# Performance work log

Measured on AMD Instinct MI355X. Metric: run time of the kernel, lower is better.

The kernel has to match this reference:

```python
import jax, jax.numpy as jnp
import numpy as np

B, S, D, H, FF = 2, 2048, 1024, 16, 4096
HD = D // H
EPS = 1e-5


def _ln(x, g, b):
    m = jnp.mean(x, axis=-1, keepdims=True)
    v = jnp.mean((x - m) ** 2, axis=-1, keepdims=True)
    return (x - m) * jax.lax.rsqrt(v + EPS) * g + b


def _rope(x, cos, sin):
    # non-standard RoPE: split full d_model at half, rotate (pre head-split)
    half = x.shape[-1] // 2
    x1, x2 = x[..., :half], x[..., half:]
    return jnp.concatenate([x1 * cos - x2 * sin, x1 * sin + x2 * cos], axis=-1)


def _heads(x, b, s):
    return x.reshape(b, s, H, HD).transpose(0, 2, 1, 3)  # [b,h,s,hd]


def _attn(q, k, v):
    scores = jnp.einsum('bhqd,bhkd->bhqk', q, k) / jnp.sqrt(jnp.float32(HD))
    w = jax.nn.softmax(scores, axis=-1)
    return jnp.einsum('bhqk,bhkd->bhqd', w, v)


def setup_inputs() -> dict:
    key = jax.random.key(0)
    ks = jax.random.split(key, 32)
    sc = 0.02
    d = {
        'x': jax.random.normal(ks[0], (B, S, D), jnp.float32),
        'cond_emb': jax.random.normal(ks[1], (B, D), jnp.float32),
    }
    # proper RoPE tables over half_dim = D//2
    pos = np.arange(S)[:, None]
    inv = 1.0 / (10000.0 ** (np.arange(D // 2) / (D // 2)))
    ang = pos * inv[None, :]
    d['cos_pos'] = jnp.asarray(np.cos(ang), jnp.float32)
    d['sin_pos'] = jnp.asarray(np.sin(ang), jnp.float32)
    names = ['Wq', 'Wk', 'Wv', 'Wo', 'Wqc', 'Wkc', 'Wvc', 'Woc']
    for i, n in enumerate(names):
        d[n] = jax.random.normal(ks[2 + i], (D, D), jnp.float32) * sc
        d['b' + n[1:]] = jnp.zeros((D,), jnp.float32)
    d['W1'] = jax.random.normal(ks[12], (D, FF), jnp.float32) * sc
    d['b1'] = jnp.zeros((FF,), jnp.float32)
    d['W2'] = jax.random.normal(ks[13], (FF, D), jnp.float32) * sc
    d['b2'] = jnp.zeros((D,), jnp.float32)
    for i in (1, 2, 3):
        d[f'g{i}'] = jnp.ones((D,), jnp.float32)
        d[f'be{i}'] = jnp.zeros((D,), jnp.float32)
    return d


def reference(x, cond_emb, cos_pos, sin_pos,
              Wq, bq, Wk, bk, Wv, bv, Wo, bo,
              Wqc, bqc, Wkc, bkc, Wvc, bvc, Woc, boc,
              W1, b1, W2, b2, g1, be1, g2, be2, g3, be3):
    b, s, _ = x.shape
    # self-attention with RoPE applied on full d_model before head split
    residual = x
    xn = _ln(x, g1, be1)
    q = _rope(xn @ Wq + bq, cos_pos, sin_pos)
    k = _rope(xn @ Wk + bk, cos_pos, sin_pos)
    v = xn @ Wv + bv
    o = _attn(_heads(q, b, s), _heads(k, b, s), _heads(v, b, s))
    o = o.transpose(0, 2, 1, 3).reshape(b, s, D) @ Wo + bo
    x = residual + o
    # cross-attention with single-token context
    residual = x
    xn = _ln(x, g2, be2)
    cond = cond_emb[:, None, :]  # [b,1,D]
    qc = _heads(xn @ Wqc + bqc, b, s)
    kc = _heads(cond @ Wkc + bkc, b, 1)
    vc = _heads(cond @ Wvc + bvc, b, 1)
    oc = _attn(qc, kc, vc)
    oc = oc.transpose(0, 2, 1, 3).reshape(b, s, D) @ Woc + boc
    x = residual + oc
    # FFN (exact GELU)
    residual = x
    xn = _ln(x, g3, be3)
    h = jax.nn.gelu(xn @ W1 + b1, approximate=False)
    return residual + (h @ W2 + b2)
```

## Files before the change

kernel.cpp:

```cpp
#include <hip/hip_runtime.h>
#include <cmath>

#define B_  2
#define S_  2048
#define D_  1024
#define H_  16
#define HD_ 64
#define FF_ 4096
#define M_  4096

typedef __attribute__((ext_vector_type(8))) __bf16 bf16x8;
typedef __attribute__((ext_vector_type(4))) __bf16 bf16x4;
typedef __attribute__((ext_vector_type(4))) float  f32x4;

__device__ __forceinline__ void gload_lds16(void* lds, const void* g) {
    __builtin_amdgcn_global_load_lds(
        (const __attribute__((address_space(1))) unsigned int*)g,
        (__attribute__((address_space(3))) unsigned int*)lds,
        16, 0, 0);
}

#define FENCE() asm volatile("" ::: "memory")

__global__ __launch_bounds__(256)
void tcast(const float* __restrict__ src, __bf16* __restrict__ dst, int K, int N)
{
    __shared__ float t[32][33];
    int tx = threadIdx.x & 31, ty = threadIdx.x >> 5;
    int k0 = blockIdx.y * 32, n0 = blockIdx.x * 32;
#pragma unroll
    for (int i = 0; i < 4; ++i)
        t[ty + i * 8][tx] = src[(size_t)(k0 + ty + i * 8) * N + n0 + tx];
    __syncthreads();
#pragma unroll
    for (int i = 0; i < 4; ++i)
        dst[(size_t)(n0 + ty + i * 8) * K + k0 + tx] = (__bf16)t[tx][ty + i * 8];
}

__global__ __launch_bounds__(256)
void catb(const float* __restrict__ a, const float* __restrict__ b,
          const float* __restrict__ c, float* __restrict__ o)
{
    int i = blockIdx.x * 256 + threadIdx.x;
    o[i] = i < 1024 ? a[i] : (i < 2048 ? b[i - 1024] : c[i - 2048]);
}

__global__ __launch_bounds__(256)
void colgemv(const float* __restrict__ inp, const float* __restrict__ W,
             const float* __restrict__ bias, float* __restrict__ out, int K, int N)
{
    __shared__ float part[4][16];
    const int b = blockIdx.y;
    const int t = threadIdx.x;
    const int w = t >> 6, lane = t & 63;
    const int colIdx = lane & 15;
    const int col = blockIdx.x * 16 + colIdx;
    const int ks = w * 4 + (lane >> 4);
    const int kpt = K >> 4;
    const float* ip = inp + (size_t)b * K + ks * kpt;
    const float* wp = W + (size_t)ks * kpt * N + col;
    float acc = 0.f;
#pragma unroll 8
    for (int i = 0; i < kpt; ++i)
        acc += ip[i] * wp[(size_t)i * N];
    acc += __shfl_xor(acc, 16);
    acc += __shfl_xor(acc, 32);
    if (lane < 16) part[w][colIdx] = acc;
    __syncthreads();
    if (t < 16) {
        float r = part[0][t] + part[1][t] + part[2][t] + part[3][t]
                + bias[blockIdx.x * 16 + t];
        out[(size_t)b * N + blockIdx.x * 16 + t] = r;
    }
}

__global__ __launch_bounds__(256)
void ln_cast(const float* __restrict__ x, const float* __restrict__ g,
             const float* __restrict__ be, __bf16* __restrict__ out)
{
    int row = blockIdx.x, tid = threadIdx.x;
    const float4* xp = (const float4*)(x + (size_t)row * D_);
    float4 v = xp[tid];
    float s  = v.x + v.y + v.z + v.w;
    float s2 = v.x * v.x + v.y * v.y + v.z * v.z + v.w * v.w;
#pragma unroll
    for (int off = 32; off > 0; off >>= 1) {
        s  += __shfl_down(s, off);
        s2 += __shfl_down(s2, off);
    }
    __shared__ float rs[4], rs2[4];
    int wid = tid >> 6, lane = tid & 63;
    if (lane == 0) { rs[wid] = s; rs2[wid] = s2; }
    __syncthreads();
    float tot  = rs[0] + rs[1] + rs[2] + rs[3];
    float tot2 = rs2[0] + rs2[1] + rs2[2] + rs2[3];
    float mean = tot * (1.0f / D_);
    float var  = tot2 * (1.0f / D_) - mean * mean;
    float rstd = rsqrtf(var + 1e-5f);
    float4 gv = ((const float4*)g)[tid];
    float4 bv = ((const float4*)be)[tid];
    bf16x4 ov;
    ov[0] = (__bf16)((v.x - mean) * rstd * gv.x + bv.x);
    ov[1] = (__bf16)((v.y - mean) * rstd * gv.y + bv.y);
    ov[2] = (__bf16)((v.z - mean) * rstd * gv.z + bv.z);
    ov[3] = (__bf16)((v.w - mean) * rstd * gv.w + bv.w);
    ((bf16x4*)(out + (size_t)row * D_))[tid] = ov;
}

__global__ __launch_bounds__(128)
void rope2(const __bf16* __restrict__ qkv, const float* __restrict__ cosp,
           const float* __restrict__ sinp, __bf16* __restrict__ out,
           int off, float scale)
{
    int row = blockIdx.x, tid = threadIdx.x;
    int b = row >> 11, s = row & 2047;
    bf16x4 a  = *(const bf16x4*)(qkv + (size_t)row * 3072 + off + tid * 4);
    bf16x4 bb = *(const bf16x4*)(qkv + (size_t)row * 3072 + off + 512 + tid * 4);
    float4 c  = ((const float4*)(cosp + (size_t)s * 512))[tid];
    float4 sn = ((const float4*)(sinp + (size_t)s * 512))[tid];
    float x1a = (float)a[0],  x1b = (float)a[1],  x1c = (float)a[2],  x1d = (float)a[3];
    float x2a = (float)bb[0], x2b = (float)bb[1], x2c = (float)bb[2], x2d = (float)bb[3];
    int d0 = tid * 4;
    int h1 = d0 >> 6, dd = d0 & 63;
    bf16x4 o1, o2;
    o1[0] = (__bf16)((x1a * c.x - x2a * sn.x) * scale);
    o1[1] = (__bf16)((x1b * c.y - x2b * sn.y) * scale);
    o1[2] = (__bf16)((x1c * c.z - x2c * sn.z) * scale);
    o1[3] = (__bf16)((x1d * c.w - x2d * sn.w) * scale);
    o2[0] = (__bf16)((x1a * sn.x + x2a * c.x) * scale);
    o2[1] = (__bf16)((x1b * sn.y + x2b * c.y) * scale);
    o2[2] = (__bf16)((x1c * sn.z + x2c * c.z) * scale);
    o2[3] = (__bf16)((x1d * sn.w + x2d * c.w) * scale);
    *(bf16x4*)(out + ((size_t)((b * H_ + h1) * S_ + s) * HD_) + dd) = o1;
    *(bf16x4*)(out + ((size_t)((b * H_ + h1 + 8) * S_ + s) * HD_) + dd) = o2;
}

__global__ __launch_bounds__(256)
void vtrans2(const __bf16* __restrict__ qkv, __bf16* __restrict__ Vt)
{
    __shared__ __bf16 t[32][33];
    int tx = threadIdx.x & 31, ty = threadIdx.x >> 5;
    int bh = blockIdx.z;
    int b = bh >> 4, h = bh & 15;
    int s0 = blockIdx.y * 32, d0 = blockIdx.x * 32;
    __bf16* dst = Vt + (size_t)bh * HD_ * S_;
#pragma unroll
    for (int i = 0; i < 4; ++i)
        t[ty + i * 8][tx] = qkv[(size_t)(b * 2048 + s0 + ty + i * 8) * 3072
                                + 2048 + h * 64 + d0 + tx];
    __syncthreads();
#pragma unroll
    for (int i = 0; i < 4; ++i)
        dst[(size_t)(d0 + ty + i * 8) * S_ + s0 + tx] = t[tx][ty + i * 8];
}

template<int EPI>
__global__ __launch_bounds__(512)
void gemm8(const __bf16* __restrict__ A, const __bf16* __restrict__ Bt,
           const float* __restrict__ bias, __bf16* __restrict__ o0,
           __bf16* __restrict__ o1, int M, int N, int K, int klen)
{
    __shared__ __align__(16) char smem[131072];
    const int tid = threadIdx.x;
    const int wid = tid >> 6, lane = tid & 63;
    const int l15 = lane & 15, l16 = lane >> 4;
    const int wm = wid >> 2, wn = wid & 3;

    const int gx = gridDim.x;
    const int nwg = gx * gridDim.y;
    int wg = blockIdx.y * gx + blockIdx.x;
    wg = (wg & 7) * (nwg >> 3) + (wg >> 3);
    const int n0 = (wg % gx) * 256;
    const int m0 = (wg / gx) * 256;
    const int kz = blockIdx.z * klen;
    const size_t K2 = (size_t)K * 2;

    const int srow = tid >> 3;
    const int scol = ((tid & 7) * 16) ^ ((srow & 7) << 4);
    const char* gA = (const char*)A + (size_t)(m0 + srow) * K2 + (size_t)kz * 2 + scol;
    const char* gB = (const char*)Bt + (size_t)(n0 + srow) * K2 + (size_t)kz * 2 + scol;

    auto stageA = [&](int c) {
        char* d = (char*)smem + c * 32768 + wid * 1024;
        gload_lds16(d,         gA);
        gload_lds16(d + 8192,  gA + 64 * K2);
        gload_lds16(d + 16384, gA + 128 * K2);
        gload_lds16(d + 24576, gA + 192 * K2);
    };
    auto stageB = [&](int c) {
        char* d = (char*)smem + 65536 + c * 32768 + wid * 1024;
        gload_lds16(d,         gB);
        gload_lds16(d + 8192,  gB + 64 * K2);
        gload_lds16(d + 16384, gB + 128 * K2);
        gload_lds16(d + 24576, gB + 192 * K2);
    };

    const int sw = (l15 & 7) << 4;
    const int x0 = (l16 * 16) ^ sw;
    const int x1 = (64 + l16 * 16) ^ sw;
    const int aoff = (wm * 128 + l15) * 128;
    const int boff = 65536 + (wn * 64 + l15) * 128;

    f32x4 acc[8][4] = {};
    const int NT = klen >> 6;

    stageA(0); stageB(0); gA += 128; gB += 128;
    stageA(1); stageB(1); gA += 128; gB += 128;
    asm volatile("s_waitcnt vmcnt(8)" ::: "memory");
    __builtin_amdgcn_s_barrier();

    for (int t = 0; t < NT; ++t) {
        const int cur = t & 1;
        const char* sa = (const char*)smem + cur * 32768;
        const bool pf = (t + 2) < NT;

        bf16x8 af0[8], af1[8];
        bf16x8 b00, b01, b02, b03, b10, b11, b12, b13;

#pragma unroll
        for (int mi = 0; mi < 8; ++mi)
            af0[mi] = *(const bf16x8*)(sa + aoff + mi * 2048 + x0);
        b00 = *(const bf16x8*)(sa + boff + 0 * 2048 + x0);
        b01 = *(const bf16x8*)(sa + boff + 1 * 2048 + x0);
        FENCE();
        __builtin_amdgcn_s_barrier();
        __builtin_amdgcn_s_setprio(1);
#pragma unroll
        for (int mi = 0; mi < 8; ++mi) {
            acc[mi][0] = __builtin_amdgcn_mfma_f32_16x16x32_bf16(af0[mi], b00, acc[mi][0], 0, 0, 0);
            acc[mi][1] = __builtin_amdgcn_mfma_f32_16x16x32_bf16(af0[mi], b01, acc[mi][1], 0, 0, 0);
        }
        __builtin_amdgcn_s_setprio(0);

#pragma unroll
        for (int mi = 0; mi < 8; ++mi)
            af1[mi] = *(const bf16x8*)(sa + aoff + mi * 2048 + x1);
        b02 = *(const bf16x8*)(sa + boff + 2 * 2048 + x0);
        b03 = *(const bf16x8*)(sa + boff + 3 * 2048 + x0);
        FENCE();
        __builtin_amdgcn_s_barrier();
        __builtin_amdgcn_s_setprio(1);
#pragma unroll
        for (int mi = 0; mi < 8; ++mi) {
            acc[mi][2] = __builtin_amdgcn_mfma_f32_16x16x32_bf16(af0[mi], b02, acc[mi][2], 0, 0, 0);
            acc[mi][3] = __builtin_amdgcn_mfma_f32_16x16x32_bf16(af0[mi], b03, acc[mi][3], 0, 0, 0);
        }
        __builtin_amdgcn_s_setprio(0);

        b10 = *(const bf16x8*)(sa + boff + 0 * 2048 + x1);
        b11 = *(const bf16x8*)(sa + boff + 1 * 2048 + x1);
        FENCE();
        __builtin_amdgcn_s_barrier();
        if (pf) stageA(cur);
        __builtin_amdgcn_s_setprio(1);
#pragma unroll
        for (int mi = 0; mi < 8; ++mi) {
            acc[mi][0] = __builtin_amdgcn_mfma_f32_16x16x32_bf16(af1[mi], b10, acc[mi][0], 0, 0, 0);
            acc[mi][1] = __builtin_amdgcn_mfma_f32_16x16x32_bf16(af1[mi], b11, acc[mi][1], 0, 0, 0);
        }
        __builtin_amdgcn_s_setprio(0);

        b12 = *(const bf16x8*)(sa + boff + 2 * 2048 + x1);
        b13 = *(const bf16x8*)(sa + boff + 3 * 2048 + x1);
        FENCE();
        __builtin_amdgcn_s_barrier();
        if (pf) { stageB(cur); gA += 128; gB += 128; }
        __builtin_amdgcn_s_setprio(1);
#pragma unroll
        for (int mi = 0; mi < 8; ++mi) {
            acc[mi][2] = __builtin_amdgcn_mfma_f32_16x16x32_bf16(af1[mi], b12, acc[mi][2], 0, 0, 0);
            acc[mi][3] = __builtin_amdgcn_mfma_f32_16x16x32_bf16(af1[mi], b13, acc[mi][3], 0, 0, 0);
        }
        __builtin_amdgcn_s_setprio(0);
        if (pf) asm volatile("s_waitcnt vmcnt(8)" ::: "memory");
        else    asm volatile("s_waitcnt vmcnt(0)" ::: "memory");
        __builtin_amdgcn_s_barrier();
        FENCE();
    }

#pragma unroll
    for (int mi = 0; mi < 8; ++mi)
#pragma unroll
        for (int ni = 0; ni < 4; ++ni) {
            int gc = n0 + wn * 64 + ni * 16 + l15;
            float bb = (EPI == 2) ? 0.f : bias[gc];
#pragma unroll
            for (int r = 0; r < 4; ++r) {
                int gr = m0 + wm * 128 + mi * 16 + l16 * 4 + r;
                float v = acc[mi][ni][r] + bb;
                if constexpr (EPI == 0) {
                    o0[(size_t)gr * N + gc] = (__bf16)v;
                } else if constexpr (EPI == 1) {
                    o0[(size_t)gr * N + gc] =
                        (__bf16)(0.5f * v * (1.0f + erff(v * 0.70710678118f)));
                } else {
                    const size_t PSZ = (size_t)M_ * 1024;
                    __bf16* po = (blockIdx.z < 2) ? (o0 + blockIdx.z * PSZ)
                                                  : (o1 + (blockIdx.z - 2) * PSZ);
                    po[(size_t)gr * N + gc] = (__bf16)v;
                }
            }
        }
}

__global__ __launch_bounds__(256)
void ffn2_red(const __bf16* __restrict__ pA, const __bf16* __restrict__ pB,
              const float* __restrict__ x2, const float* __restrict__ b2,
              float* __restrict__ out)
{
    const size_t PSZ = (size_t)M_ * 1024;
    size_t i = ((size_t)blockIdx.x * 256 + threadIdx.x) * 8;
    bf16x8 a0 = *(const bf16x8*)(pA + i);
    bf16x8 a1 = *(const bf16x8*)(pA + PSZ + i);
    bf16x8 c0 = *(const bf16x8*)(pB + i);
    bf16x8 c1 = *(const bf16x8*)(pB + PSZ + i);
    float4 xa = *(const float4*)(x2 + i);
    float4 xb = *(const float4*)(x2 + i + 4);
    float xs[8] = {xa.x, xa.y, xa.z, xa.w, xb.x, xb.y, xb.z, xb.w};
#pragma unroll
    for (int j = 0; j < 8; ++j) {
        int col = (int)((i + j) & 1023);
        out[i + j] = xs[j] + b2[col]
                   + (float)a0[j] + (float)a1[j] + (float)c0[j] + (float)c1[j];
    }
}

__global__ __launch_bounds__(256)
void gemm_bt(const __bf16* __restrict__ A, const __bf16* __restrict__ Bt,
             const float* __restrict__ bias, const float* __restrict__ resid,
             const float* __restrict__ extra, float* __restrict__ outF,
             int M, int N, int K)
{
    __shared__ __align__(16) __bf16 As[128 * 64];
    __shared__ __align__(16) __bf16 Bs[128 * 64];
    const int tid = threadIdx.x;
    const int wid = tid >> 6, lane = tid & 63;
    const int m0 = blockIdx.y * 128, n0 = blockIdx.x * 128;
    const int wm = wid >> 1, wn = wid & 1;
    const int l15 = lane & 15, l16 = lane >> 4;

    f32x4 acc[4][4] = {};
    char* asb = (char*)As;
    char* bsb = (char*)Bs;
    const char* ag = (const char*)A;
    const char* bg = (const char*)Bt;
    const int srow = lane >> 3;
    const int scolsw = ((lane & 7) * 16) ^ (srow << 4);

    for (int k0 = 0; k0 < K; k0 += 64) {
        __syncthreads();
#pragma unroll
        for (int i = 0; i < 4; ++i) {
            int j = wid * 4 + i;
            int row = j * 8 + srow;
            gload_lds16(asb + j * 1024,
                        ag + (size_t)(m0 + row) * (K * 2) + k0 * 2 + scolsw);
        }
#pragma unroll
        for (int i = 0; i < 4; ++i) {
            int j = wid * 4 + i;
            int row = j * 8 + srow;
            gload_lds16(bsb + j * 1024,
                        bg + (size_t)(n0 + row) * (K * 2) + k0 * 2 + scolsw);
        }
        __syncthreads();

        bf16x8 af[4][2], bfr[4][2];
#pragma unroll
        for (int mi = 0; mi < 4; ++mi) {
            int row = wm * 64 + mi * 16 + l15;
            int swl = (row & 7) << 4;
#pragma unroll
            for (int kk = 0; kk < 2; ++kk)
                af[mi][kk] = *(const bf16x8*)(asb + row * 128 + ((l16 * 16 + kk * 64) ^ swl));
        }
#pragma unroll
        for (int ni = 0; ni < 4; ++ni) {
            int row = wn * 64 + ni * 16 + l15;
            int swl = (row & 7) << 4;
#pragma unroll
            for (int kk = 0; kk < 2; ++kk)
                bfr[ni][kk] = *(const bf16x8*)(bsb + row * 128 + ((l16 * 16 + kk * 64) ^ swl));
        }
#pragma unroll
        for (int mi = 0; mi < 4; ++mi)
#pragma unroll
            for (int ni = 0; ni < 4; ++ni) {
                acc[mi][ni] = __builtin_amdgcn_mfma_f32_16x16x32_bf16(af[mi][0], bfr[ni][0], acc[mi][ni], 0, 0, 0);
                acc[mi][ni] = __builtin_amdgcn_mfma_f32_16x16x32_bf16(af[mi][1], bfr[ni][1], acc[mi][ni], 0, 0, 0);
            }
    }

#pragma unroll
    for (int mi = 0; mi < 4; ++mi)
#pragma unroll
        for (int ni = 0; ni < 4; ++ni) {
            int gc = n0 + wn * 64 + ni * 16 + l15;
            float bb = bias[gc];
#pragma unroll
            for (int r = 0; r < 4; ++r) {
                int gr = m0 + wm * 64 + mi * 16 + l16 * 4 + r;
                float v = acc[mi][ni][r] + bb;
                size_t idx = (size_t)gr * N + gc;
                int b = gr >> 11;
                outF[idx] = resid[idx] + v + extra[(size_t)b * N + gc];
            }
        }
}

__global__ __launch_bounds__(256)
void attn_fwd(const __bf16* __restrict__ Qh, const __bf16* __restrict__ Kh,
              const __bf16* __restrict__ Vt, __bf16* __restrict__ O)
{
    __shared__ __align__(16) char smem[24576];
    char* Kl = smem;
    char* Vl = smem + 8192;
    char* Pl = smem + 16384;
    const int tid = threadIdx.x, wid = tid >> 6, lane = tid & 63;
    const int l15 = lane & 15, l16 = lane >> 4;
    const int bh = blockIdx.y;
    const int q0 = blockIdx.x * 64 + wid * 16;
    const size_t qkbase = (size_t)bh * S_ * HD_;

    bf16x8 qf[2];
    {
        const __bf16* qp = Qh + qkbase + (size_t)(q0 + l15) * HD_ + l16 * 8;
        qf[0] = *(const bf16x8*)qp;
        qf[1] = *(const bf16x8*)(qp + 32);
    }
    float m = -1e30f, sum = 0.f;
    f32x4 o[4] = {};
    const int srow = lane >> 3;
    const int scolsw = ((lane & 7) * 16) ^ (srow << 4);
    const char* kg = (const char*)(Kh + qkbase);
    const char* vg = (const char*)(Vt + (size_t)bh * HD_ * S_);

    for (int kt = 0; kt < S_ / 64; ++kt) {
        int s0 = kt * 64;
        __syncthreads();
#pragma unroll
        for (int c = 0; c < 2; ++c) {
            int j = wid * 2 + c;
            int row = j * 8 + srow;
            gload_lds16(Kl + j * 1024, kg + (size_t)(s0 + row) * 128 + scolsw);
            gload_lds16(Vl + j * 1024, vg + (size_t)row * (S_ * 2) + s0 * 2 + scolsw);
        }
        __syncthreads();

        f32x4 st[4];
#pragma unroll
        for (int t = 0; t < 4; ++t) {
            int row = t * 16 + l15;
            int swl = (row & 7) << 4;
            bf16x8 ak0 = *(const bf16x8*)(Kl + row * 128 + ((l16 * 16) ^ swl));
            bf16x8 ak1 = *(const bf16x8*)(Kl + row * 128 + ((l16 * 16 + 64) ^ swl));
            f32x4 z = {0.f, 0.f, 0.f, 0.f};
            z = __builtin_amdgcn_mfma_f32_16x16x32_bf16(ak0, qf[0], z, 0, 0, 0);
            st[t] = __builtin_amdgcn_mfma_f32_16x16x32_bf16(ak1, qf[1], z, 0, 0, 0);
        }
        float rmax = -1e30f;
#pragma unroll
        for (int t = 0; t < 4; ++t)
#pragma unroll
            for (int r = 0; r < 4; ++r) rmax = fmaxf(rmax, st[t][r]);
        rmax = fmaxf(rmax, __shfl_xor(rmax, 16));
        rmax = fmaxf(rmax, __shfl_xor(rmax, 32));
        float mnew = fmaxf(m, rmax);
        float corr = __expf(m - mnew);
        float rsum = 0.f;
        float p[4][4];
#pragma unroll
        for (int t = 0; t < 4; ++t)
#pragma unroll
            for (int r = 0; r < 4; ++r) { p[t][r] = __expf(st[t][r] - mnew); rsum += p[t][r]; }
        rsum += __shfl_xor(rsum, 16);
        rsum += __shfl_xor(rsum, 32);
        sum = sum * corr + rsum;
        m = mnew;
        {
            char* pw = Pl + wid * 2048 + l15 * 128;
            int swl = (l15 & 7) << 4;
#pragma unroll
            for (int t = 0; t < 4; ++t) {
                bf16x4 pk;
                pk[0] = (__bf16)p[t][0]; pk[1] = (__bf16)p[t][1];
                pk[2] = (__bf16)p[t][2]; pk[3] = (__bf16)p[t][3];
                *(bf16x4*)(pw + ((t * 32 + l16 * 8) ^ swl)) = pk;
            }
        }
        float c0 = __shfl(corr, l16 * 4 + 0);
        float c1 = __shfl(corr, l16 * 4 + 1);
        float c2 = __shfl(corr, l16 * 4 + 2);
        float c3 = __shfl(corr, l16 * 4 + 3);
#pragma unroll
        for (int dg = 0; dg < 4; ++dg) {
            o[dg][0] *= c0; o[dg][1] *= c1; o[dg][2] *= c2; o[dg][3] *= c3;
        }
        {
            const char* pr = Pl + wid * 2048 + l15 * 128;
            int swp = (l15 & 7) << 4;
            bf16x8 ap0 = *(const bf16x8*)(pr + ((l16 * 16) ^ swp));
            bf16x8 ap1 = *(const bf16x8*)(pr + ((l16 * 16 + 64) ^ swp));
#pragma unroll
            for (int dg = 0; dg < 4; ++dg) {
                int row = dg * 16 + l15;
                int swl = (row & 7) << 4;
                bf16x8 bv0 = *(const bf16x8*)(Vl + row * 128 + ((l16 * 16) ^ swl));
                bf16x8 bv1 = *(const bf16x8*)(Vl + row * 128 + ((l16 * 16 + 64) ^ swl));
                o[dg] = __builtin_amdgcn_mfma_f32_16x16x32_bf16(ap0, bv0, o[dg], 0, 0, 0);
                o[dg] = __builtin_amdgcn_mfma_f32_16x16x32_bf16(ap1, bv1, o[dg], 0, 0, 0);
            }
        }
    }
    int b = bh >> 4, hh = bh & 15;
#pragma unroll
    for (int r = 0; r < 4; ++r) {
        float inv = 1.0f / __shfl(sum, l16 * 4 + r);
        int qg = q0 + l16 * 4 + r;
        __bf16* op = O + ((size_t)(b * S_ + qg) * D_) + hh * HD_;
#pragma unroll
        for (int dg = 0; dg < 4; ++dg)
            op[dg * 16 + l15] = (__bf16)(o[dg][r] * inv);
    }
}

extern "C" void kernel_launch(void* const* d_in, const int* in_sizes, int n_in,
                              void* d_out, int out_size, void* d_ws, size_t ws_size,
                              hipStream_t stream)
{
    (void)in_sizes; (void)n_in; (void)out_size; (void)ws_size;
    const float* x    = (const float*)d_in[0];
    const float* cond = (const float*)d_in[1];
    const float* cosp = (const float*)d_in[2];
    const float* sinp = (const float*)d_in[3];
    const float* Wq = (const float*)d_in[4];  const float* bq = (const float*)d_in[5];
    const float* Wk = (const float*)d_in[6];  const float* bk = (const float*)d_in[7];
    const float* Wv = (const float*)d_in[8];  const float* bv = (const float*)d_in[9];
    const float* Wo = (const float*)d_in[10]; const float* bo = (const float*)d_in[11];
    const float* Wvc = (const float*)d_in[16]; const float* bvc = (const float*)d_in[17];
    const float* Woc = (const float*)d_in[18]; const float* boc = (const float*)d_in[19];
    const float* W1 = (const float*)d_in[20]; const float* b1 = (const float*)d_in[21];
    const float* W2 = (const float*)d_in[22]; const float* b2 = (const float*)d_in[23];
    const float* g1 = (const float*)d_in[24]; const float* be1 = (const float*)d_in[25];
    const float* g3 = (const float*)d_in[28]; const float* be3 = (const float*)d_in[29];

    char* ws = (char*)d_ws;
    const size_t MB = 1ull << 20;
    __bf16* WqkvT = (__bf16*)(ws + 0 * MB);
    __bf16* WoT   = (__bf16*)(ws + 6 * MB);
    __bf16* W1T   = (__bf16*)(ws + 8 * MB);
    __bf16* W2T   = (__bf16*)(ws + 16 * MB);
    __bf16* xn    = (__bf16*)(ws + 24 * MB);
    __bf16* qkvh  = (__bf16*)(ws + 32 * MB);
    __bf16* Qh    = (__bf16*)(ws + 56 * MB);
    __bf16* Kh    = (__bf16*)(ws + 64 * MB);
    __bf16* Vt    = (__bf16*)(ws + 72 * MB);
    __bf16* oflat = (__bf16*)(ws + 80 * MB);
    float*  bqkv  = (float*)(ws + 88 * MB);
    float*  vc    = (float*)(ws + 88 * MB + 16384);
    float*  ocp   = (float*)(ws + 88 * MB + 32768);
    float*  x2    = (float*)(ws + 32 * MB);
    __bf16* hbuf  = (__bf16*)(ws + 48 * MB);
    __bf16* pA    = (__bf16*)(ws + 0 * MB);
    __bf16* pB    = (__bf16*)(ws + 80 * MB);

    tcast<<<dim3(32, 32),  256, 0, stream>>>(Wq, WqkvT,                 1024, 1024);
    tcast<<<dim3(32, 32),  256, 0, stream>>>(Wk, WqkvT + 1024 * 1024,   1024, 1024);
    tcast<<<dim3(32, 32),  256, 0, stream>>>(Wv, WqkvT + 2048 * 1024,   1024, 1024);
    tcast<<<dim3(32, 32),  256, 0, stream>>>(Wo, WoT, 1024, 1024);
    tcast<<<dim3(128, 32), 256, 0, stream>>>(W1, W1T, 1024, 4096);
    tcast<<<dim3(32, 128), 256, 0, stream>>>(W2, W2T, 4096, 1024);
    catb<<<12, 256, 0, stream>>>(bq, bk, bv, bqkv);
    colgemv<<<dim3(64, 2), 256, 0, stream>>>(cond, Wvc, bvc, vc, 1024, 1024);
    colgemv<<<dim3(64, 2), 256, 0, stream>>>(vc, Woc, boc, ocp, 1024, 1024);
    ln_cast<<<M_, 256, 0, stream>>>(x, g1, be1, xn);
    gemm8<0><<<dim3(12, 16, 1), 512, 0, stream>>>(xn, WqkvT, bqkv, qkvh, nullptr,
                                                  M_, 3072, 1024, 1024);
    rope2<<<M_, 128, 0, stream>>>(qkvh, cosp, sinp, Qh, 0, 0.125f);
    rope2<<<M_, 128, 0, stream>>>(qkvh, cosp, sinp, Kh, 1024, 1.0f);
    vtrans2<<<dim3(2, 64, 32), 256, 0, stream>>>(qkvh, Vt);
    attn_fwd<<<dim3(32, 32), 256, 0, stream>>>(Qh, Kh, Vt, oflat);
    gemm_bt<<<dim3(8, 32), 256, 0, stream>>>(oflat, WoT, bo, x, ocp, x2,
                                             M_, 1024, 1024);
    ln_cast<<<M_, 256, 0, stream>>>(x2, g3, be3, xn);
    gemm8<1><<<dim3(16, 16, 1), 512, 0, stream>>>(xn, W1T, b1, hbuf, nullptr,
                                                  M_, 4096, 1024, 1024);
    gemm8<2><<<dim3(4, 16, 4), 512, 0, stream>>>(hbuf, W2T, nullptr, pA, pB,
                                                 M_, 1024, 4096, 1024);
    ffn2_red<<<2048, 256, 0, stream>>>(pA, pB, x2, b2, (float*)d_out);
}
```

Baseline: 286.9 us.

## Double-buffer attention K/V loads, add lazy rescale, and merge small kernels

After: 274.3 us. 4.4% less time.

```diff
diff --git a/kernel.cpp b/kernel.cpp
--- a/kernel.cpp
+++ b/kernel.cpp
@@ -35,6 +35,24 @@
 #pragma unroll
     for (int i = 0; i < 4; ++i)
         dst[(size_t)(n0 + ty + i * 8) * K + k0 + tx] = (__bf16)t[tx][ty + i * 8];
+}
+
+__global__ __launch_bounds__(256)
+void tcast3(const float* __restrict__ wa, const float* __restrict__ wb,
+            const float* __restrict__ wc, __bf16* __restrict__ dstb)
+{
+    __shared__ float t[32][33];
+    const float* src = blockIdx.z == 0 ? wa : (blockIdx.z == 1 ? wb : wc);
+    __bf16* dst = dstb + (size_t)blockIdx.z * 1024 * 1024;
+    int tx = threadIdx.x & 31, ty = threadIdx.x >> 5;
+    int k0 = blockIdx.y * 32, n0 = blockIdx.x * 32;
+#pragma unroll
+    for (int i = 0; i < 4; ++i)
+        t[ty + i * 8][tx] = src[(size_t)(k0 + ty + i * 8) * 1024 + n0 + tx];
+    __syncthreads();
+#pragma unroll
+    for (int i = 0; i < 4; ++i)
+        dst[(size_t)(n0 + ty + i * 8) * 1024 + k0 + tx] = (__bf16)t[tx][ty + i * 8];
 }
 
 __global__ __launch_bounds__(256)
@@ -108,31 +126,37 @@
 }
 
 __global__ __launch_bounds__(128)
-void rope2(const __bf16* __restrict__ qkv, const float* __restrict__ cosp,
-           const float* __restrict__ sinp, __bf16* __restrict__ out,
-           int off, float scale)
+void rope_qk(const __bf16* __restrict__ qkv, const float* __restrict__ cosp,
+             const float* __restrict__ sinp, __bf16* __restrict__ Qh,
+             __bf16* __restrict__ Kh)
 {
     int row = blockIdx.x, tid = threadIdx.x;
     int b = row >> 11, s = row & 2047;
-    bf16x4 a  = *(const bf16x4*)(qkv + (size_t)row * 3072 + off + tid * 4);
-    bf16x4 bb = *(const bf16x4*)(qkv + (size_t)row * 3072 + off + 512 + tid * 4);
     float4 c  = ((const float4*)(cosp + (size_t)s * 512))[tid];
     float4 sn = ((const float4*)(sinp + (size_t)s * 512))[tid];
-    float x1a = (float)a[0],  x1b = (float)a[1],  x1c = (float)a[2],  x1d = (float)a[3];
-    float x2a = (float)bb[0], x2b = (float)bb[1], x2c = (float)bb[2], x2d = (float)bb[3];
     int d0 = tid * 4;
     int h1 = d0 >> 6, dd = d0 & 63;
-    bf16x4 o1, o2;
-    o1[0] = (__bf16)((x1a * c.x - x2a * sn.x) * scale);
-    o1[1] = (__bf16)((x1b * c.y - x2b * sn.y) * scale);
-    o1[2] = (__bf16)((x1c * c.z - x2c * sn.z) * scale);
-    o1[3] = (__bf16)((x1d * c.w - x2d * sn.w) * scale);
-    o2[0] = (__bf16)((x1a * sn.x + x2a * c.x) * scale);
-    o2[1] = (__bf16)((x1b * sn.y + x2b * c.y) * scale);
-    o2[2] = (__bf16)((x1c * sn.z + x2c * c.z) * scale);
-    o2[3] = (__bf16)((x1d * sn.w + x2d * c.w) * scale);
-    *(bf16x4*)(out + ((size_t)((b * H_ + h1) * S_ + s) * HD_) + dd) = o1;
-    *(bf16x4*)(out + ((size_t)((b * H_ + h1 + 8) * S_ + s) * HD_) + dd) = o2;
+#pragma unroll
+    for (int which = 0; which < 2; ++which) {
+        const int off = which * 1024;
+        const float scale = which ? 1.0f : 0.125f;
+        __bf16* out = which ? Kh : Qh;
+        bf16x4 a  = *(const bf16x4*)(qkv + (size_t)row * 3072 + off + tid * 4);
+        bf16x4 bb = *(const bf16x4*)(qkv + (size_t)row * 3072 + off + 512 + tid * 4);
+        float x1a = (float)a[0],  x1b = (float)a[1],  x1c = (float)a[2],  x1d = (float)a[3];
+        float x2a = (float)bb[0], x2b = (float)bb[1], x2c = (float)bb[2], x2d = (float)bb[3];
+        bf16x4 o1, o2;
+        o1[0] = (__bf16)((x1a * c.x - x2a * sn.x) * scale);
+        o1[1] = (__bf16)((x1b * c.y - x2b * sn.y) * scale);
+        o1[2] = (__bf16)((x1c * c.z - x2c * sn.z) * scale);
+        o1[3] = (__bf16)((x1d * c.w - x2d * sn.w) * scale);
+        o2[0] = (__bf16)((x1a * sn.x + x2a * c.x) * scale);
+        o2[1] = (__bf16)((x1b * sn.y + x2b * c.y) * scale);
+        o2[2] = (__bf16)((x1c * sn.z + x2c * c.z) * scale);
+        o2[3] = (__bf16)((x1d * sn.w + x2d * c.w) * scale);
+        *(bf16x4*)(out + ((size_t)((b * H_ + h1) * S_ + s) * HD_) + dd) = o1;
+        *(bf16x4*)(out + ((size_t)((b * H_ + h1 + 8) * S_ + s) * HD_) + dd) = o2;
+    }
 }
 
 __global__ __launch_bounds__(256)
@@ -412,14 +436,16 @@
 void attn_fwd(const __bf16* __restrict__ Qh, const __bf16* __restrict__ Kh,
               const __bf16* __restrict__ Vt, __bf16* __restrict__ O)
 {
-    __shared__ __align__(16) char smem[24576];
-    char* Kl = smem;
-    char* Vl = smem + 8192;
-    char* Pl = smem + 16384;
+    __shared__ __align__(16) char smem[40960];
     const int tid = threadIdx.x, wid = tid >> 6, lane = tid & 63;
     const int l15 = lane & 15, l16 = lane >> 4;
-    const int bh = blockIdx.y;
-    const int q0 = blockIdx.x * 64 + wid * 16;
+
+    const int wg = blockIdx.x;
+    const int rr = wg >> 3;
+    const int qb = rr & 31;
+    const int bh = (wg & 7) + 8 * (rr >> 5);
+
+    const int q0 = qb * 64 + wid * 16;
     const size_t qkbase = (size_t)bh * S_ * HD_;
 
     bf16x8 qf[2];
@@ -435,19 +461,33 @@
     const char* kg = (const char*)(Kh + qkbase);
     const char* vg = (const char*)(Vt + (size_t)bh * HD_ * S_);
 
-    for (int kt = 0; kt < S_ / 64; ++kt) {
-        int s0 = kt * 64;
-        __syncthreads();
-#pragma unroll
-        for (int c = 0; c < 2; ++c) {
-            int j = wid * 2 + c;
+    auto stage = [&](int c, int t) {
+        int s0 = t * 64;
+#pragma unroll
+        for (int cc = 0; cc < 2; ++cc) {
+            int j = wid * 2 + cc;
             int row = j * 8 + srow;
-            gload_lds16(Kl + j * 1024, kg + (size_t)(s0 + row) * 128 + scolsw);
-            gload_lds16(Vl + j * 1024, vg + (size_t)row * (S_ * 2) + s0 * 2 + scolsw);
-        }
-        __syncthreads();
+            gload_lds16(smem + c * 8192 + j * 1024,
+                        kg + (size_t)(s0 + row) * 128 + scolsw);
+            gload_lds16(smem + 16384 + c * 8192 + j * 1024,
+                        vg + (size_t)row * (S_ * 2) + s0 * 2 + scolsw);
+        }
+    };
+
+    const int NT = S_ / 64;
+    stage(0, 0);
+    stage(1, 1);
+    asm volatile("s_waitcnt vmcnt(4)" ::: "memory");
+    __builtin_amdgcn_s_barrier();
+
+    for (int kt = 0; kt < NT; ++kt) {
+        const int cur = kt & 1;
+        const char* Kl = smem + cur * 8192;
+        const char* Vl = smem + 16384 + cur * 8192;
+        char* Pl = smem + 32768;
 
         f32x4 st[4];
+        __builtin_amdgcn_s_setprio(1);
 #pragma unroll
         for (int t = 0; t < 4; ++t) {
             int row = t * 16 + l15;
@@ -458,6 +498,8 @@
             z = __builtin_amdgcn_mfma_f32_16x16x32_bf16(ak0, qf[0], z, 0, 0, 0);
             st[t] = __builtin_amdgcn_mfma_f32_16x16x32_bf16(ak1, qf[1], z, 0, 0, 0);
         }
+        __builtin_amdgcn_s_setprio(0);
+
         float rmax = -1e30f;
 #pragma unroll
         for (int t = 0; t < 4; ++t)
@@ -465,18 +507,30 @@
             for (int r = 0; r < 4; ++r) rmax = fmaxf(rmax, st[t][r]);
         rmax = fmaxf(rmax, __shfl_xor(rmax, 16));
         rmax = fmaxf(rmax, __shfl_xor(rmax, 32));
-        float mnew = fmaxf(m, rmax);
-        float corr = __expf(m - mnew);
+        if (!__all(rmax <= m + 8.f)) {
+            float mnew = fmaxf(m, rmax);
+            float corr = __expf(m - mnew);
+            sum *= corr;
+            float c0 = __shfl(corr, l16 * 4 + 0);
+            float c1 = __shfl(corr, l16 * 4 + 1);
+            float c2 = __shfl(corr, l16 * 4 + 2);
+            float c3 = __shfl(corr, l16 * 4 + 3);
+#pragma unroll
+            for (int dg = 0; dg < 4; ++dg) {
+                o[dg][0] *= c0; o[dg][1] *= c1; o[dg][2] *= c2; o[dg][3] *= c3;
+            }
+            m = mnew;
+        }
         float rsum = 0.f;
         float p[4][4];
 #pragma unroll
         for (int t = 0; t < 4; ++t)
 #pragma unroll
-            for (int r = 0; r < 4; ++r) { p[t][r] = __expf(st[t][r] - mnew); rsum += p[t][r]; }
+            for (int r = 0; r < 4; ++r) { p[t][r] = __expf(st[t][r] - m); rsum += p[t][r]; }
         rsum += __shfl_xor(rsum, 16);
         rsum += __shfl_xor(rsum, 32);
-        sum = sum * corr + rsum;
-        m = mnew;
+        sum += rsum;
+
         {
             char* pw = Pl + wid * 2048 + l15 * 128;
             int swl = (l15 & 7) << 4;
@@ -488,19 +542,12 @@
                 *(bf16x4*)(pw + ((t * 32 + l16 * 8) ^ swl)) = pk;
             }
         }
-        float c0 = __shfl(corr, l16 * 4 + 0);
-        float c1 = __shfl(corr, l16 * 4 + 1);
-        float c2 = __shfl(corr, l16 * 4 + 2);
-        float c3 = __shfl(corr, l16 * 4 + 3);
-#pragma unroll
-        for (int dg = 0; dg < 4; ++dg) {
-            o[dg][0] *= c0; o[dg][1] *= c1; o[dg][2] *= c2; o[dg][3] *= c3;
-        }
         {
             const char* pr = Pl + wid * 2048 + l15 * 128;
             int swp = (l15 & 7) << 4;
             bf16x8 ap0 = *(const bf16x8*)(pr + ((l16 * 16) ^ swp));
             bf16x8 ap1 = *(const bf16x8*)(pr + ((l16 * 16 + 64) ^ swp));
+            __builtin_amdgcn_s_setprio(1);
 #pragma unroll
             for (int dg = 0; dg < 4; ++dg) {
                 int row = dg * 16 + l15;
@@ -510,8 +557,21 @@
                 o[dg] = __builtin_amdgcn_mfma_f32_16x16x32_bf16(ap0, bv0, o[dg], 0, 0, 0);
                 o[dg] = __builtin_amdgcn_mfma_f32_16x16x32_bf16(ap1, bv1, o[dg], 0, 0, 0);
             }
-        }
-    }
+            __builtin_amdgcn_s_setprio(0);
+        }
+
+        FENCE();
+        __builtin_amdgcn_s_barrier();
+        if (kt + 2 < NT) {
+            stage(cur, kt + 2);
+            asm volatile("s_waitcnt vmcnt(4)" ::: "memory");
+        } else {
+            asm volatile("s_waitcnt vmcnt(0)" ::: "memory");
+        }
+        __builtin_amdgcn_s_barrier();
+        FENCE();
+    }
+
     int b = bh >> 4, hh = bh & 15;
 #pragma unroll
     for (int r = 0; r < 4; ++r) {
@@ -564,9 +624,7 @@
     __bf16* pA    = (__bf16*)(ws + 0 * MB);
     __bf16* pB    = (__bf16*)(ws + 80 * MB);
 
-    tcast<<<dim3(32, 32),  256, 0, stream>>>(Wq, WqkvT,                 1024, 1024);
-    tcast<<<dim3(32, 32),  256, 0, stream>>>(Wk, WqkvT + 1024 * 1024,   1024, 1024);
-    tcast<<<dim3(32, 32),  256, 0, stream>>>(Wv, WqkvT + 2048 * 1024,   1024, 1024);
+    tcast3<<<dim3(32, 32, 3), 256, 0, stream>>>(Wq, Wk, Wv, WqkvT);
     tcast<<<dim3(32, 32),  256, 0, stream>>>(Wo, WoT, 1024, 1024);
     tcast<<<dim3(128, 32), 256, 0, stream>>>(W1, W1T, 1024, 4096);
     tcast<<<dim3(32, 128), 256, 0, stream>>>(W2, W2T, 4096, 1024);
@@ -576,10 +634,9 @@
     ln_cast<<<M_, 256, 0, stream>>>(x, g1, be1, xn);
     gemm8<0><<<dim3(12, 16, 1), 512, 0, stream>>>(xn, WqkvT, bqkv, qkvh, nullptr,
                                                   M_, 3072, 1024, 1024);
-    rope2<<<M_, 128, 0, stream>>>(qkvh, cosp, sinp, Qh, 0, 0.125f);
-    rope2<<<M_, 128, 0, stream>>>(qkvh, cosp, sinp, Kh, 1024, 1.0f);
+    rope_qk<<<M_, 128, 0, stream>>>(qkvh, cosp, sinp, Qh, Kh);
     vtrans2<<<dim3(2, 64, 32), 256, 0, stream>>>(qkvh, Vt);
-    attn_fwd<<<dim3(32, 32), 256, 0, stream>>>(Qh, Kh, Vt, oflat);
+    attn_fwd<<<1024, 256, 0, stream>>>(Qh, Kh, Vt, oflat);
     gemm_bt<<<dim3(8, 32), 256, 0, stream>>>(oflat, WoT, bo, x, ocp, x2,
                                              M_, 1024, 1024);
     ln_cast<<<M_, 256, 0, stream>>>(x2, g3, be3, xn);
```
